# Optimization experiments

Measured on AMD Instinct MI355X. Metric: run time of the kernel, lower is better.

Reference implementation:

```python
import jax, jax.numpy as jnp
import numpy as np

B, D, R, E, L = 16384, 1024, 64, 4, 3


def setup_inputs() -> dict:
    key = jax.random.key(0)
    ks = jax.random.split(key, 6)
    x0 = jax.random.normal(ks[0], (B, D), dtype=jnp.float32)
    # Expert low-rank factors: U projects D->R, V projects R->D (both bias-free)
    U = jax.random.normal(ks[1], (L, E, D, R), dtype=jnp.float32) * (1.0 / np.sqrt(D))
    V = jax.random.normal(ks[2], (L, E, R, D), dtype=jnp.float32) * (1.0 / np.sqrt(R))
    # Gate Linear(D, E) with bias
    gW = jax.random.normal(ks[3], (L, D, E), dtype=jnp.float32) * (1.0 / np.sqrt(D))
    gb = jax.random.normal(ks[4], (L, E), dtype=jnp.float32) * 0.01
    # Per-layer bias added after mixing (initialized zeros in torch; small random here)
    bias = jax.random.normal(ks[5], (L, D), dtype=jnp.float32) * 0.01
    return {"x0": x0, "U": U, "V": V, "gW": gW, "gb": gb, "bias": bias}


def reference(x0, U, V, gW, gb, bias):
    x = x0
    for l in range(L):
        # batched low-rank expert MLPs: [B,D] -> [B,E,R] -> relu -> [B,E,D]
        h = jax.nn.relu(jnp.einsum('bd,edr->ber', x, U[l]))
        expert_out = jnp.einsum('ber,erd->bed', h, V[l])
        # soft gate over experts
        gate = jax.nn.softmax(x @ gW[l] + gb[l], axis=-1)  # [B,E]
        mixed = jnp.einsum('be,bed->bd', gate, expert_out)  # [B,D]
        x = x0 * mixed + bias[l] + x
    return x
```

## Files before the change

kernel.cpp:

```cpp
#include <hip/hip_runtime.h>

#define DEVI __device__ __forceinline__

typedef __bf16 bf16x8 __attribute__((ext_vector_type(8)));
typedef float f32x4 __attribute__((ext_vector_type(4)));
typedef unsigned short u16x8 __attribute__((ext_vector_type(8)));

DEVI unsigned short f2bf(float f) {
  unsigned u = __builtin_bit_cast(unsigned, f);
  u += 0x7FFFu + ((u >> 16) & 1u);
  return (unsigned short)(u >> 16);
}
DEVI float bf2f(unsigned short h) {
  return __builtin_bit_cast(float, (unsigned)h << 16);
}


__global__ __launch_bounds__(256) void cast_x0_kernel(const float* __restrict__ x,
                                                      unsigned short* __restrict__ xb) {
  int i = blockIdx.x * 256 + threadIdx.x;
  const f32x4* p = (const f32x4*)x;
  f32x4 a = p[2 * i], b = p[2 * i + 1];
  u16x8 o;
  o[0] = f2bf(a[0]); o[1] = f2bf(a[1]); o[2] = f2bf(a[2]); o[3] = f2bf(a[3]);
  o[4] = f2bf(b[0]); o[5] = f2bf(b[1]); o[6] = f2bf(b[2]); o[7] = f2bf(b[3]);
  ((u16x8*)xb)[i] = o;
}

__global__ __launch_bounds__(256) void pack_w1_kernel(const float* __restrict__ U,
                                                      unsigned short* __restrict__ W1T) {
  int idx = blockIdx.x * 256 + threadIdx.x;
  int l = idx >> 18;
  int rem = idx & 262143;
  int n = rem >> 10, k = rem & 1023;
  int e = n >> 6, r = n & 63;
  W1T[idx] = f2bf(U[(size_t)(((l * 4 + e) << 10) + k) * 64 + r]);
}

__global__ __launch_bounds__(256) void pack_v2_kernel(const float* __restrict__ V,
                                                      unsigned short* __restrict__ V2T) {
  int idx = blockIdx.x * 256 + threadIdx.x;
  int l = idx >> 18;
  int rem = idx & 262143;
  int d = rem >> 8, c = rem & 255;
  int e = c >> 6, r = c & 63;
  V2T[idx] = f2bf(V[(size_t)(((l * 4 + e) * 64 + r) << 10) + d]);
}

__global__ __launch_bounds__(256) void pack_gw_kernel(const float* __restrict__ gW,
                                                      unsigned short* __restrict__ gWT) {
  int idx = blockIdx.x * 256 + threadIdx.x;
  int l = idx >> 14;
  int n = (idx >> 10) & 15;
  int k = idx & 1023;
  float v = (n < 4) ? gW[l * 4096 + k * 4 + n] : 0.0f;
  gWT[idx] = f2bf(v);
}

__global__ __launch_bounds__(256) void k1_kernel(const unsigned short* __restrict__ A,
                                                 const unsigned short* __restrict__ Bw,
                                                 const unsigned short* __restrict__ gWT,
                                                 const float* __restrict__ gb,
                                                 unsigned short* __restrict__ Hg) {
  constexpr int K = 1024;
  __shared__ char lds[20480];
  __shared__ float gls[128];
  int t = threadIdx.x;
  int wid = t >> 6, lane = t & 63;
  int g4 = lane >> 4, l15 = lane & 15;
  int wm = wid >> 1, wn = wid & 1;
  int m0 = blockIdx.x * 32, n0 = blockIdx.y * 128;

  int srow = t >> 3;
  int scolb = ((t & 7) * 16) ^ ((srow & 7) << 4);
  const unsigned short* Asrc = A + (size_t)(m0 + srow) * K + (scolb >> 1);
  const unsigned short* Bsrc = Bw + (size_t)(n0 + srow) * K + (scolb >> 1);

  f32x4 acc[4], accg;
  {
    f32x4 z = {0.f, 0.f, 0.f, 0.f};
    accg = z;
#pragma unroll
    for (int n = 0; n < 4; ++n) acc[n] = z;
  }

  for (int ks = 0; ks < K; ks += 64) {
    __syncthreads();
    __builtin_amdgcn_global_load_lds(
        (const __attribute__((address_space(1))) void*)(Asrc + ks),
        (__attribute__((address_space(3))) void*)(lds + wid * 1024), 16, 0, 0);
#pragma unroll
    for (int i = 0; i < 4; ++i)
      __builtin_amdgcn_global_load_lds(
          (const __attribute__((address_space(1))) void*)(Bsrc + (size_t)i * 32 * K + ks),
          (__attribute__((address_space(3))) void*)(lds + 4096 + i * 4096 + wid * 1024), 16, 0, 0);
    __syncthreads();
#pragma unroll
    for (int kk = 0; kk < 2; ++kk) {
      bf16x8 af;
      {
        int row = wm * 16 + l15;
        af = *(const bf16x8*)(lds + row * 128 + ((kk * 64 + g4 * 16) ^ ((row & 7) << 4)));
      }
      bf16x8 gf;
      if (wn == 0) gf = *(const bf16x8*)(gWT + (size_t)l15 * 1024 + ks + kk * 32 + g4 * 8);
#pragma unroll
      for (int n = 0; n < 4; ++n) {
        int row = wn * 64 + n * 16 + l15;
        bf16x8 bfr = *(const bf16x8*)(lds + 4096 + row * 128 +
                                      ((kk * 64 + g4 * 16) ^ ((row & 7) << 4)));
        acc[n] = __builtin_amdgcn_mfma_f32_16x16x32_bf16(af, bfr, acc[n], 0, 0, 0);
      }
      if (wn == 0)
        accg = __builtin_amdgcn_mfma_f32_16x16x32_bf16(af, gf, accg, 0, 0, 0);
    }
  }

  if (wn == 0) {
    float gbv = gb[l15 & 3];
#pragma unroll
    for (int j = 0; j < 4; ++j) {
      float v = accg[j] + gbv;
      float mx = fmaxf(v, __shfl_xor(v, 1));
      mx = fmaxf(mx, __shfl_xor(mx, 2));
      float ev = __expf(v - mx);
      float s = ev + __shfl_xor(ev, 1);
      s += __shfl_xor(s, 2);
      if (l15 < 4) gls[(wm * 16 + g4 * 4 + j) * 4 + l15] = ev / s;
    }
  }
  __syncthreads();

  int e = blockIdx.y * 2 + wn;
#pragma unroll
  for (int n = 0; n < 4; ++n) {
#pragma unroll
    for (int j = 0; j < 4; ++j) {
      int row = wm * 16 + g4 * 4 + j;
      int col = wn * 64 + n * 16 + l15;
      float v = fmaxf(acc[n][j], 0.f) * gls[row * 4 + e];
      *(unsigned short*)(lds + 4096 + row * 256 + ((col * 2) ^ ((row & 7) << 4))) = f2bf(v);
    }
  }
  __syncthreads();

#pragma unroll
  for (int i = 0; i < 2; ++i) {
    int row = i * 16 + (t >> 4);
    int seg = (t & 15) * 16;
    u16x8 v = *(const u16x8*)(lds + 4096 + row * 256 + (seg ^ ((row & 7) << 4)));
    *(u16x8*)(Hg + (size_t)(m0 + row) * 256 + n0 + (seg >> 1)) = v;
  }
}

__global__ __launch_bounds__(256) void k2_kernel(const unsigned short* __restrict__ A,
                                                 const unsigned short* __restrict__ Bw,
                                                 const unsigned short* __restrict__ x0b,
                                                 const float* __restrict__ x0f,
                                                 const unsigned short* __restrict__ xcur,
                                                 const float* __restrict__ biasl,
                                                 unsigned short* __restrict__ xnext,
                                                 float* __restrict__ out,
                                                 int last, int use_x0b) {
  constexpr int K = 256;
  __shared__ char lds[24576];
  int t = threadIdx.x;
  int wid = t >> 6, lane = t & 63;
  int g4 = lane >> 4, l15 = lane & 15;
  int wm = wid >> 1, wn = wid & 1;
  int m0 = blockIdx.x * 64, n0 = blockIdx.y * 128;

  int srow = t >> 3;
  int scolb = ((t & 7) * 16) ^ ((srow & 7) << 4);
  const unsigned short* Asrc = A + (size_t)(m0 + srow) * K + (scolb >> 1);
  const unsigned short* Bsrc = Bw + (size_t)(n0 + srow) * K + (scolb >> 1);

  f32x4 acc[2][4];
#pragma unroll
  for (int m = 0; m < 2; ++m)
#pragma unroll
    for (int n = 0; n < 4; ++n) { f32x4 z = {0.f, 0.f, 0.f, 0.f}; acc[m][n] = z; }

  for (int ks = 0; ks < K; ks += 64) {
    __syncthreads();
#pragma unroll
    for (int i = 0; i < 2; ++i)
      __builtin_amdgcn_global_load_lds(
          (const __attribute__((address_space(1))) void*)(Asrc + (size_t)i * 32 * K + ks),
          (__attribute__((address_space(3))) void*)(lds + i * 4096 + wid * 1024), 16, 0, 0);
#pragma unroll
    for (int i = 0; i < 4; ++i)
      __builtin_amdgcn_global_load_lds(
          (const __attribute__((address_space(1))) void*)(Bsrc + (size_t)i * 32 * K + ks),
          (__attribute__((address_space(3))) void*)(lds + 8192 + i * 4096 + wid * 1024), 16, 0, 0);
    __syncthreads();
#pragma unroll
    for (int kk = 0; kk < 2; ++kk) {
      bf16x8 af[2];
#pragma unroll
      for (int m = 0; m < 2; ++m) {
        int row = wm * 32 + m * 16 + l15;
        af[m] = *(const bf16x8*)(lds + row * 128 + ((kk * 64 + g4 * 16) ^ ((row & 7) << 4)));
      }
#pragma unroll
      for (int n = 0; n < 4; ++n) {
        int row = wn * 64 + n * 16 + l15;
        bf16x8 bfr = *(const bf16x8*)(lds + 8192 + row * 128 +
                                      ((kk * 64 + g4 * 16) ^ ((row & 7) << 4)));
#pragma unroll
        for (int m = 0; m < 2; ++m)
          acc[m][n] = __builtin_amdgcn_mfma_f32_16x16x32_bf16(af[m], bfr, acc[m][n], 0, 0, 0);
      }
    }
  }
  __syncthreads();

#pragma unroll
  for (int m = 0; m < 2; ++m) {
#pragma unroll
    for (int n = 0; n < 4; ++n) {
#pragma unroll
      for (int j = 0; j < 4; ++j) {
        int row = wm * 32 + m * 16 + g4 * 4 + j;
        int col = wn * 64 + n * 16 + l15;
        *(unsigned short*)(lds + 8192 + row * 256 + ((col * 2) ^ ((row & 7) << 4))) =
            f2bf(acc[m][n][j]);
      }
    }
  }
  __syncthreads();

#pragma unroll
  for (int i = 0; i < 4; ++i) {
    int row = i * 16 + (t >> 4);
    int seg = (t & 15) * 16;
    u16x8 a8 = *(const u16x8*)(lds + 8192 + row * 256 + (seg ^ ((row & 7) << 4)));
    size_t goff = (size_t)(m0 + row) * 1024 + n0 + (seg >> 1);
    u16x8 cv = *(const u16x8*)(xcur + goff);
    float x0v[8];
    if (use_x0b) {
      u16x8 xv = *(const u16x8*)(x0b + goff);
#pragma unroll
      for (int k = 0; k < 8; ++k) x0v[k] = bf2f(xv[k]);
    } else {
      f32x4 xa = *(const f32x4*)(x0f + goff);
      f32x4 xb2 = *(const f32x4*)(x0f + goff + 4);
#pragma unroll
      for (int k = 0; k < 4; ++k) { x0v[k] = xa[k]; x0v[k + 4] = xb2[k]; }
    }
    const float* bp = biasl + n0 + (seg >> 1);
    f32x4 b0 = *(const f32x4*)bp;
    f32x4 b1 = *(const f32x4*)(bp + 4);
    float r[8];
#pragma unroll
    for (int k = 0; k < 8; ++k) {
      float bv = (k < 4) ? b0[k & 3] : b1[k & 3];
      r[k] = x0v[k] * bf2f(a8[k]) + bv + bf2f(cv[k]);
    }
    if (last) {
      f32x4 r0, r1;
#pragma unroll
      for (int k = 0; k < 4; ++k) { r0[k] = r[k]; r1[k] = r[k + 4]; }
      *(f32x4*)(out + goff) = r0;
      *(f32x4*)(out + goff + 4) = r1;
    } else {
      u16x8 o;
#pragma unroll
      for (int k = 0; k < 8; ++k) o[k] = f2bf(r[k]);
      *(u16x8*)(xnext + goff) = o;
    }
  }
}

extern "C" void kernel_launch(void* const* d_in, const int* in_sizes, int n_in,
                              void* d_out, int out_size, void* d_ws, size_t ws_size,
                              hipStream_t stream) {
  const float* x0 = (const float*)d_in[0];
  const float* U = (const float*)d_in[1];
  const float* V = (const float*)d_in[2];
  const float* gW = (const float*)d_in[3];
  const float* gb = (const float*)d_in[4];
  const float* bias = (const float*)d_in[5];
  float* out = (float*)d_out;
  char* ws = (char*)d_ws;

  const size_t SZ_X = 33554432;
  const size_t SZ_HG = 8388608;
  const size_t SZ_W = 1572864;
  const size_t SZ_GW = 98304;
  bool use_x0b = ws_size >= (2 * SZ_X + SZ_HG + 2 * SZ_W + SZ_GW);

  size_t off = 0;
  unsigned short* x0b = nullptr;
  if (use_x0b) { x0b = (unsigned short*)(ws + off); off += SZ_X; }
  unsigned short* xbf = (unsigned short*)(ws + off); off += SZ_X;
  unsigned short* hg = (unsigned short*)(ws + off); off += SZ_HG;
  unsigned short* W1T = (unsigned short*)(ws + off); off += SZ_W;
  unsigned short* V2T = (unsigned short*)(ws + off); off += SZ_W;
  unsigned short* gWT = (unsigned short*)(ws + off); off += SZ_GW;

  unsigned short* xinit = use_x0b ? x0b : xbf;

  cast_x0_kernel<<<8192, 256, 0, stream>>>(x0, xinit);
  pack_w1_kernel<<<3072, 256, 0, stream>>>(U, W1T);
  pack_v2_kernel<<<3072, 256, 0, stream>>>(V, V2T);
  pack_gw_kernel<<<192, 256, 0, stream>>>(gW, gWT);

  for (int l = 0; l < 3; ++l) {
    const unsigned short* xs = (l == 0) ? xinit : xbf;
    k1_kernel<<<dim3(512, 2), 256, 0, stream>>>(xs, W1T + l * 262144, gWT + l * 16384,
                                                gb + l * 4, hg);
    k2_kernel<<<dim3(256, 8), 256, 0, stream>>>(hg, V2T + l * 262144,
                                                use_x0b ? x0b : nullptr, x0, xs,
                                                bias + l * 1024, xbf, out,
                                                (l == 2) ? 1 : 0, use_x0b ? 1 : 0);
  }
}
```

Before: 180.8 us.

## Retile k1 to cover all 256 columns per block and shrink k2 M tile

k1 now gives each block all 256 output columns (4 experts × 64 rank), one expert per wave. The A tile of x is then loaded once per 32-row tile instead of twice, and the gate GEMM and softmax run once per row tile instead of per column half. k2 is cut from 64-row to 32-row tiles, which doubles its grid to spread the small-K GEMM and epilogue across more blocks. The trade-off is that k1 needs more LDS and has half as many blocks, while k2 reloads the V weights more often.

```diff
diff --git a/kernel.cpp b/kernel.cpp
--- a/kernel.cpp
+++ b/kernel.cpp
@@ -63,25 +63,25 @@
                                                  const float* __restrict__ gb,
                                                  unsigned short* __restrict__ Hg) {
   constexpr int K = 1024;
-  __shared__ char lds[20480];
+  __shared__ char lds[36864];
   __shared__ float gls[128];
   int t = threadIdx.x;
   int wid = t >> 6, lane = t & 63;
   int g4 = lane >> 4, l15 = lane & 15;
-  int wm = wid >> 1, wn = wid & 1;
-  int m0 = blockIdx.x * 32, n0 = blockIdx.y * 128;
+  int m0 = blockIdx.x * 32;
 
   int srow = t >> 3;
   int scolb = ((t & 7) * 16) ^ ((srow & 7) << 4);
   const unsigned short* Asrc = A + (size_t)(m0 + srow) * K + (scolb >> 1);
-  const unsigned short* Bsrc = Bw + (size_t)(n0 + srow) * K + (scolb >> 1);
-
-  f32x4 acc[4], accg;
-  {
+  const unsigned short* Bsrc = Bw + (size_t)srow * K + (scolb >> 1);
+
+  f32x4 acc[2][4], accg[2];
+#pragma unroll
+  for (int m = 0; m < 2; ++m) {
     f32x4 z = {0.f, 0.f, 0.f, 0.f};
-    accg = z;
-#pragma unroll
-    for (int n = 0; n < 4; ++n) acc[n] = z;
+    accg[m] = z;
+#pragma unroll
+    for (int n = 0; n < 4; ++n) acc[m][n] = z;
   }
 
   for (int ks = 0; ks < K; ks += 64) {
@@ -90,66 +90,77 @@
         (const __attribute__((address_space(1))) void*)(Asrc + ks),
         (__attribute__((address_space(3))) void*)(lds + wid * 1024), 16, 0, 0);
 #pragma unroll
-    for (int i = 0; i < 4; ++i)
+    for (int i = 0; i < 8; ++i)
       __builtin_amdgcn_global_load_lds(
           (const __attribute__((address_space(1))) void*)(Bsrc + (size_t)i * 32 * K + ks),
           (__attribute__((address_space(3))) void*)(lds + 4096 + i * 4096 + wid * 1024), 16, 0, 0);
     __syncthreads();
 #pragma unroll
     for (int kk = 0; kk < 2; ++kk) {
-      bf16x8 af;
-      {
-        int row = wm * 16 + l15;
-        af = *(const bf16x8*)(lds + row * 128 + ((kk * 64 + g4 * 16) ^ ((row & 7) << 4)));
+      bf16x8 af[2];
+#pragma unroll
+      for (int m = 0; m < 2; ++m) {
+        int row = m * 16 + l15;
+        af[m] = *(const bf16x8*)(lds + row * 128 + ((kk * 64 + g4 * 16) ^ ((row & 7) << 4)));
       }
       bf16x8 gf;
-      if (wn == 0) gf = *(const bf16x8*)(gWT + (size_t)l15 * 1024 + ks + kk * 32 + g4 * 8);
+      if (wid == 0) gf = *(const bf16x8*)(gWT + (size_t)l15 * 1024 + ks + kk * 32 + g4 * 8);
 #pragma unroll
       for (int n = 0; n < 4; ++n) {
-        int row = wn * 64 + n * 16 + l15;
+        int row = wid * 64 + n * 16 + l15;
         bf16x8 bfr = *(const bf16x8*)(lds + 4096 + row * 128 +
                                       ((kk * 64 + g4 * 16) ^ ((row & 7) << 4)));
-        acc[n] = __builtin_amdgcn_mfma_f32_16x16x32_bf16(af, bfr, acc[n], 0, 0, 0);
-      }
-      if (wn == 0)
-        accg = __builtin_amdgcn_mfma_f32_16x16x32_bf16(af, gf, accg, 0, 0, 0);
-    }
-  }
-
-  if (wn == 0) {
+#pragma unroll
+        for (int m = 0; m < 2; ++m)
+          acc[m][n] = __builtin_amdgcn_mfma_f32_16x16x32_bf16(af[m], bfr, acc[m][n], 0, 0, 0);
+      }
+      if (wid == 0) {
+#pragma unroll
+        for (int m = 0; m < 2; ++m)
+          accg[m] = __builtin_amdgcn_mfma_f32_16x16x32_bf16(af[m], gf, accg[m], 0, 0, 0);
+      }
+    }
+  }
+
+  if (wid == 0) {
     float gbv = gb[l15 & 3];
 #pragma unroll
-    for (int j = 0; j < 4; ++j) {
-      float v = accg[j] + gbv;
-      float mx = fmaxf(v, __shfl_xor(v, 1));
-      mx = fmaxf(mx, __shfl_xor(mx, 2));
-      float ev = __expf(v - mx);
-      float s = ev + __shfl_xor(ev, 1);
-      s += __shfl_xor(s, 2);
-      if (l15 < 4) gls[(wm * 16 + g4 * 4 + j) * 4 + l15] = ev / s;
+    for (int m = 0; m < 2; ++m) {
+#pragma unroll
+      for (int j = 0; j < 4; ++j) {
+        float v = accg[m][j] + gbv;
+        float mx = fmaxf(v, __shfl_xor(v, 1));
+        mx = fmaxf(mx, __shfl_xor(mx, 2));
+        float ev = __expf(v - mx);
+        float s = ev + __shfl_xor(ev, 1);
+        s += __shfl_xor(s, 2);
+        if (l15 < 4) gls[(m * 16 + g4 * 4 + j) * 4 + l15] = ev / s;
+      }
     }
   }
   __syncthreads();
 
-  int e = blockIdx.y * 2 + wn;
-#pragma unroll
-  for (int n = 0; n < 4; ++n) {
-#pragma unroll
-    for (int j = 0; j < 4; ++j) {
-      int row = wm * 16 + g4 * 4 + j;
-      int col = wn * 64 + n * 16 + l15;
-      float v = fmaxf(acc[n][j], 0.f) * gls[row * 4 + e];
-      *(unsigned short*)(lds + 4096 + row * 256 + ((col * 2) ^ ((row & 7) << 4))) = f2bf(v);
+#pragma unroll
+  for (int m = 0; m < 2; ++m) {
+#pragma unroll
+    for (int n = 0; n < 4; ++n) {
+#pragma unroll
+      for (int j = 0; j < 4; ++j) {
+        int row = m * 16 + g4 * 4 + j;
+        int col = wid * 64 + n * 16 + l15;
+        float v = fmaxf(acc[m][n][j], 0.f) * gls[row * 4 + wid];
+        *(unsigned short*)(lds + 4096 + row * 512 + ((col * 2) ^ ((row & 7) << 4))) = f2bf(v);
+      }
     }
   }
   __syncthreads();
 
 #pragma unroll
-  for (int i = 0; i < 2; ++i) {
-    int row = i * 16 + (t >> 4);
-    int seg = (t & 15) * 16;
-    u16x8 v = *(const u16x8*)(lds + 4096 + row * 256 + (seg ^ ((row & 7) << 4)));
-    *(u16x8*)(Hg + (size_t)(m0 + row) * 256 + n0 + (seg >> 1)) = v;
+  for (int i = 0; i < 4; ++i) {
+    int row = i * 8 + (t >> 5);
+    int seg = (t & 31) * 16;
+    u16x8 v = *(const u16x8*)(lds + 4096 + row * 512 + (seg ^ ((row & 7) << 4)));
+    *(u16x8*)(Hg + (size_t)(m0 + row) * 256 + (seg >> 1)) = v;
   }
 }
 
@@ -163,78 +174,68 @@
                                                  float* __restrict__ out,
                                                  int last, int use_x0b) {
   constexpr int K = 256;
-  __shared__ char lds[24576];
+  __shared__ char lds[20480];
   int t = threadIdx.x;
   int wid = t >> 6, lane = t & 63;
   int g4 = lane >> 4, l15 = lane & 15;
   int wm = wid >> 1, wn = wid & 1;
-  int m0 = blockIdx.x * 64, n0 = blockIdx.y * 128;
+  int m0 = blockIdx.x * 32, n0 = blockIdx.y * 128;
 
   int srow = t >> 3;
   int scolb = ((t & 7) * 16) ^ ((srow & 7) << 4);
   const unsigned short* Asrc = A + (size_t)(m0 + srow) * K + (scolb >> 1);
   const unsigned short* Bsrc = Bw + (size_t)(n0 + srow) * K + (scolb >> 1);
 
-  f32x4 acc[2][4];
-#pragma unroll
-  for (int m = 0; m < 2; ++m)
-#pragma unroll
-    for (int n = 0; n < 4; ++n) { f32x4 z = {0.f, 0.f, 0.f, 0.f}; acc[m][n] = z; }
+  f32x4 acc[4];
+#pragma unroll
+  for (int n = 0; n < 4; ++n) { f32x4 z = {0.f, 0.f, 0.f, 0.f}; acc[n] = z; }
 
   for (int ks = 0; ks < K; ks += 64) {
     __syncthreads();
-#pragma unroll
-    for (int i = 0; i < 2; ++i)
-      __builtin_amdgcn_global_load_lds(
-          (const __attribute__((address_space(1))) void*)(Asrc + (size_t)i * 32 * K + ks),
-          (__attribute__((address_space(3))) void*)(lds + i * 4096 + wid * 1024), 16, 0, 0);
+    __builtin_amdgcn_global_load_lds(
+        (const __attribute__((address_space(1))) void*)(Asrc + ks),
+        (__attribute__((address_space(3))) void*)(lds + wid * 1024), 16, 0, 0);
 #pragma unroll
     for (int i = 0; i < 4; ++i)
       __builtin_amdgcn_global_load_lds(
           (const __attribute__((address_space(1))) void*)(Bsrc + (size_t)i * 32 * K + ks),
-          (__attribute__((address_space(3))) void*)(lds + 8192 + i * 4096 + wid * 1024), 16, 0, 0);
+          (__attribute__((address_space(3))) void*)(lds + 4096 + i * 4096 + wid * 1024), 16, 0, 0);
     __syncthreads();
 #pragma unroll
     for (int kk = 0; kk < 2; ++kk) {
-      bf16x8 af[2];
-#pragma unroll
-      for (int m = 0; m < 2; ++m) {
-        int row = wm * 32 + m * 16 + l15;
-        af[m] = *(const bf16x8*)(lds + row * 128 + ((kk * 64 + g4 * 16) ^ ((row & 7) << 4)));
+      bf16x8 af;
+      {
+        int row = wm * 16 + l15;
+        af = *(const bf16x8*)(lds + row * 128 + ((kk * 64 + g4 * 16) ^ ((row & 7) << 4)));
       }
 #pragma unroll
       for (int n = 0; n < 4; ++n) {
         int row = wn * 64 + n * 16 + l15;
-        bf16x8 bfr = *(const bf16x8*)(lds + 8192 + row * 128 +
+        bf16x8 bfr = *(const bf16x8*)(lds + 4096 + row * 128 +
                                       ((kk * 64 + g4 * 16) ^ ((row & 7) << 4)));
-#pragma unroll
-        for (int m = 0; m < 2; ++m)
-          acc[m][n] = __builtin_amdgcn_mfma_f32_16x16x32_bf16(af[m], bfr, acc[m][n], 0, 0, 0);
+        acc[n] = __builtin_amdgcn_mfma_f32_16x16x32_bf16(af, bfr, acc[n], 0, 0, 0);
       }
     }
   }
   __syncthreads();
 
 #pragma unroll
-  for (int m = 0; m < 2; ++m) {
-#pragma unroll
-    for (int n = 0; n < 4; ++n) {
-#pragma unroll
-      for (int j = 0; j < 4; ++j) {
-        int row = wm * 32 + m * 16 + g4 * 4 + j;
-        int col = wn * 64 + n * 16 + l15;
-        *(unsigned short*)(lds + 8192 + row * 256 + ((col * 2) ^ ((row & 7) << 4))) =
-            f2bf(acc[m][n][j]);
-      }
+  for (int n = 0; n < 4; ++n) {
+#pragma unroll
+    for (int j = 0; j < 4; ++j) {
+      int row = wm * 16 + g4 * 4 + j;
+      int col = wn * 64 + n * 16 + l15;
+      *(unsigned short*)(lds + 4096 + row * 256 + ((col * 2) ^ ((row & 7) << 4))) =
+          f2bf(acc[n][j]);
     }
   }
   __syncthreads();
 
 #pragma unroll
-  for (int i = 0; i < 4; ++i) {
+  for (int i = 0; i < 2; ++i) {
     int row = i * 16 + (t >> 4);
     int seg = (t & 15) * 16;
-    u16x8 a8 = *(const u16x8*)(lds + 8192 + row * 256 + (seg ^ ((row & 7) << 4)));
+    u16x8 a8 = *(const u16x8*)(lds + 4096 + row * 256 + (seg ^ ((row & 7) << 4)));
     size_t goff = (size_t)(m0 + row) * 1024 + n0 + (seg >> 1);
     u16x8 cv = *(const u16x8*)(xcur + goff);
     float x0v[8];
@@ -248,7 +249,7 @@
 #pragma unroll
       for (int k = 0; k < 4; ++k) { x0v[k] = xa[k]; x0v[k + 4] = xb2[k]; }
     }
-    const float* bp = biasl + n0 + (seg >> 1);
+    const float* bp = biasl + n0 + ((seg >> 1));
     f32x4 b0 = *(const f32x4*)bp;
     f32x4 b1 = *(const f32x4*)(bp + 4);
     float r[8];
@@ -308,9 +309,9 @@
 
   for (int l = 0; l < 3; ++l) {
     const unsigned short* xs = (l == 0) ? xinit : xbf;
-    k1_kernel<<<dim3(512, 2), 256, 0, stream>>>(xs, W1T + l * 262144, gWT + l * 16384,
-                                                gb + l * 4, hg);
-    k2_kernel<<<dim3(256, 8), 256, 0, stream>>>(hg, V2T + l * 262144,
+    k1_kernel<<<512, 256, 0, stream>>>(xs, W1T + l * 262144, gWT + l * 16384,
+                                       gb + l * 4, hg);
+    k2_kernel<<<dim3(512, 8), 256, 0, stream>>>(hg, V2T + l * 262144,
                                                 use_x0b ? x0b : nullptr, x0, xs,
                                                 bias + l * 1024, xbf, out,
                                                 (l == 2) ? 1 : 0, use_x0b ? 1 : 0);
```

Result: slower. 185.3 us (+2.5%).

## Load k2 operands straight to registers and retile to 32x256 blocks

Applied to the files above, without the earlier changes.

The second GEMM kernel no longer stages A and B tiles through LDS with global_load_lds and block-wide barriers. Each wave keeps its full 32-row K=256 slice of the gated hidden activations in registers and streams V2T fragments directly from global memory into MFMAs. The block tile changes from 64x128 to 32x256 with per-wave 64-column strips, which removes the main-loop synchronisation and shrinks LDS use. In exchange it raises register pressure and relies on L2 and L1 for reuse of V2T across blocks, with no LDS-level sharing of operands between waves.

```diff
diff --git a/kernel.cpp b/kernel.cpp
--- a/kernel.cpp
+++ b/kernel.cpp
@@ -153,8 +153,8 @@
   }
 }
 
-__global__ __launch_bounds__(256) void k2_kernel(const unsigned short* __restrict__ A,
-                                                 const unsigned short* __restrict__ Bw,
+__global__ __launch_bounds__(256) void k2_kernel(const unsigned short* __restrict__ hg,
+                                                 const unsigned short* __restrict__ V2T,
                                                  const unsigned short* __restrict__ x0b,
                                                  const float* __restrict__ x0f,
                                                  const unsigned short* __restrict__ xcur,
@@ -162,79 +162,58 @@
                                                  unsigned short* __restrict__ xnext,
                                                  float* __restrict__ out,
                                                  int last, int use_x0b) {
-  constexpr int K = 256;
-  __shared__ char lds[24576];
+  __shared__ char lds[16384];
   int t = threadIdx.x;
   int wid = t >> 6, lane = t & 63;
   int g4 = lane >> 4, l15 = lane & 15;
-  int wm = wid >> 1, wn = wid & 1;
-  int m0 = blockIdx.x * 64, n0 = blockIdx.y * 128;
-
-  int srow = t >> 3;
-  int scolb = ((t & 7) * 16) ^ ((srow & 7) << 4);
-  const unsigned short* Asrc = A + (size_t)(m0 + srow) * K + (scolb >> 1);
-  const unsigned short* Bsrc = Bw + (size_t)(n0 + srow) * K + (scolb >> 1);
+  int m0 = blockIdx.y * 32;
+  int n0 = blockIdx.x * 256 + wid * 64;
+
+  bf16x8 a[2][8];
+#pragma unroll
+  for (int mm = 0; mm < 2; ++mm) {
+    const unsigned short* ar = hg + (size_t)(m0 + mm * 16 + l15) * 256 + g4 * 8;
+#pragma unroll
+    for (int kc = 0; kc < 8; ++kc) a[mm][kc] = *(const bf16x8*)(ar + kc * 32);
+  }
 
   f32x4 acc[2][4];
 #pragma unroll
-  for (int m = 0; m < 2; ++m)
-#pragma unroll
-    for (int n = 0; n < 4; ++n) { f32x4 z = {0.f, 0.f, 0.f, 0.f}; acc[m][n] = z; }
-
-  for (int ks = 0; ks < K; ks += 64) {
-    __syncthreads();
-#pragma unroll
-    for (int i = 0; i < 2; ++i)
-      __builtin_amdgcn_global_load_lds(
-          (const __attribute__((address_space(1))) void*)(Asrc + (size_t)i * 32 * K + ks),
-          (__attribute__((address_space(3))) void*)(lds + i * 4096 + wid * 1024), 16, 0, 0);
-#pragma unroll
-    for (int i = 0; i < 4; ++i)
-      __builtin_amdgcn_global_load_lds(
-          (const __attribute__((address_space(1))) void*)(Bsrc + (size_t)i * 32 * K + ks),
-          (__attribute__((address_space(3))) void*)(lds + 8192 + i * 4096 + wid * 1024), 16, 0, 0);
-    __syncthreads();
-#pragma unroll
-    for (int kk = 0; kk < 2; ++kk) {
-      bf16x8 af[2];
-#pragma unroll
-      for (int m = 0; m < 2; ++m) {
-        int row = wm * 32 + m * 16 + l15;
-        af[m] = *(const bf16x8*)(lds + row * 128 + ((kk * 64 + g4 * 16) ^ ((row & 7) << 4)));
+  for (int mm = 0; mm < 2; ++mm)
+#pragma unroll
+    for (int n = 0; n < 4; ++n) { f32x4 z = {0.f, 0.f, 0.f, 0.f}; acc[mm][n] = z; }
+
+#pragma unroll
+  for (int kc = 0; kc < 8; ++kc) {
+#pragma unroll
+    for (int n = 0; n < 4; ++n) {
+      bf16x8 b = *(const bf16x8*)(V2T + (size_t)(n0 + n * 16 + l15) * 256 + kc * 32 + g4 * 8);
+#pragma unroll
+      for (int mm = 0; mm < 2; ++mm)
+        acc[mm][n] = __builtin_amdgcn_mfma_f32_16x16x32_bf16(a[mm][kc], b, acc[mm][n], 0, 0, 0);
+    }
+  }
+
+  char* wlds = lds + wid * 4096;
+#pragma unroll
+  for (int mm = 0; mm < 2; ++mm) {
+#pragma unroll
+    for (int n = 0; n < 4; ++n) {
+#pragma unroll
+      for (int j = 0; j < 4; ++j) {
+        int row = mm * 16 + g4 * 4 + j;
+        int colb = (n * 16 + l15) * 2;
+        *(unsigned short*)(wlds + row * 128 + (colb ^ ((row & 3) << 5))) = f2bf(acc[mm][n][j]);
       }
-#pragma unroll
-      for (int n = 0; n < 4; ++n) {
-        int row = wn * 64 + n * 16 + l15;
-        bf16x8 bfr = *(const bf16x8*)(lds + 8192 + row * 128 +
-                                      ((kk * 64 + g4 * 16) ^ ((row & 7) << 4)));
-#pragma unroll
-        for (int m = 0; m < 2; ++m)
-          acc[m][n] = __builtin_amdgcn_mfma_f32_16x16x32_bf16(af[m], bfr, acc[m][n], 0, 0, 0);
-      }
     }
   }
   __syncthreads();
 
 #pragma unroll
-  for (int m = 0; m < 2; ++m) {
-#pragma unroll
-    for (int n = 0; n < 4; ++n) {
-#pragma unroll
-      for (int j = 0; j < 4; ++j) {
-        int row = wm * 32 + m * 16 + g4 * 4 + j;
-        int col = wn * 64 + n * 16 + l15;
-        *(unsigned short*)(lds + 8192 + row * 256 + ((col * 2) ^ ((row & 7) << 4))) =
-            f2bf(acc[m][n][j]);
-      }
-    }
-  }
-  __syncthreads();
-
-#pragma unroll
-  for (int i = 0; i < 4; ++i) {
-    int row = i * 16 + (t >> 4);
-    int seg = (t & 15) * 16;
-    u16x8 a8 = *(const u16x8*)(lds + 8192 + row * 256 + (seg ^ ((row & 7) << 4)));
+  for (int p = 0; p < 4; ++p) {
+    int row = p * 8 + (lane >> 3);
+    int seg = (lane & 7) * 16;
+    u16x8 a8 = *(const u16x8*)(wlds + row * 128 + (seg ^ ((row & 3) << 5)));
     size_t goff = (size_t)(m0 + row) * 1024 + n0 + (seg >> 1);
     u16x8 cv = *(const u16x8*)(xcur + goff);
     float x0v[8];
@@ -310,7 +289,7 @@
     const unsigned short* xs = (l == 0) ? xinit : xbf;
     k1_kernel<<<dim3(512, 2), 256, 0, stream>>>(xs, W1T + l * 262144, gWT + l * 16384,
                                                 gb + l * 4, hg);
-    k2_kernel<<<dim3(256, 8), 256, 0, stream>>>(hg, V2T + l * 262144,
+    k2_kernel<<<dim3(4, 512), 256, 0, stream>>>(hg, V2T + l * 262144,
                                                 use_x0b ? x0b : nullptr, x0, xs,
                                                 bias + l * 1024, xbf, out,
                                                 (l == 2) ? 1 : 0, use_x0b ? 1 : 0);
```

After: 284.0 us. 57.1% more time.

## Double-buffer LDS tiles in both GEMM kernels to overlap loads with MFMA

Applied to the files above, without the earlier changes.

Both GEMM main loops now use two LDS buffers. The next K-slice is issued via global_load_lds before the MFMAs on the current slice run, and there is one barrier per iteration instead of two. The aim is to hide global-to-LDS latency behind compute. In exchange, LDS per block doubles (about 40 KB and 48 KB), which can cut the number of resident blocks per CU.

```diff
diff --git a/kernel.cpp b/kernel.cpp
--- a/kernel.cpp
+++ b/kernel.cpp
@@ -63,7 +63,7 @@
                                                  const float* __restrict__ gb,
                                                  unsigned short* __restrict__ Hg) {
   constexpr int K = 1024;
-  __shared__ char lds[20480];
+  __shared__ char lds[40960];
   __shared__ float gls[128];
   int t = threadIdx.x;
   int wid = t >> 6, lane = t & 63;
@@ -84,37 +84,48 @@
     for (int n = 0; n < 4; ++n) acc[n] = z;
   }
 
-  for (int ks = 0; ks < K; ks += 64) {
-    __syncthreads();
-    __builtin_amdgcn_global_load_lds(
-        (const __attribute__((address_space(1))) void*)(Asrc + ks),
-        (__attribute__((address_space(3))) void*)(lds + wid * 1024), 16, 0, 0);
-#pragma unroll
-    for (int i = 0; i < 4; ++i)
-      __builtin_amdgcn_global_load_lds(
-          (const __attribute__((address_space(1))) void*)(Bsrc + (size_t)i * 32 * K + ks),
-          (__attribute__((address_space(3))) void*)(lds + 4096 + i * 4096 + wid * 1024), 16, 0, 0);
-    __syncthreads();
+#define K1_STAGE(b, ks)                                                                       \
+  {                                                                                           \
+    __builtin_amdgcn_global_load_lds(                                                         \
+        (const __attribute__((address_space(1))) void*)(Asrc + (ks)),                         \
+        (__attribute__((address_space(3))) void*)(lds + (b)*20480 + wid * 1024), 16, 0, 0);   \
+    _Pragma("unroll") for (int i = 0; i < 4; ++i) __builtin_amdgcn_global_load_lds(           \
+        (const __attribute__((address_space(1))) void*)(Bsrc + (size_t)i * 32 * K + (ks)),    \
+        (__attribute__((address_space(3))) void*)(lds + (b)*20480 + 4096 + i * 4096 +         \
+                                                  wid * 1024),                                \
+        16, 0, 0);                                                                            \
+  }
+
+  int cur = 0;
+  K1_STAGE(0, 0);
+  __syncthreads();
+
+  for (int s = 0; s < 16; ++s) {
+    if (s < 15) K1_STAGE(cur ^ 1, (s + 1) * 64);
+    const char* base = lds + cur * 20480;
 #pragma unroll
     for (int kk = 0; kk < 2; ++kk) {
       bf16x8 af;
       {
         int row = wm * 16 + l15;
-        af = *(const bf16x8*)(lds + row * 128 + ((kk * 64 + g4 * 16) ^ ((row & 7) << 4)));
+        af = *(const bf16x8*)(base + row * 128 + ((kk * 64 + g4 * 16) ^ ((row & 7) << 4)));
       }
       bf16x8 gf;
-      if (wn == 0) gf = *(const bf16x8*)(gWT + (size_t)l15 * 1024 + ks + kk * 32 + g4 * 8);
+      if (wn == 0) gf = *(const bf16x8*)(gWT + (size_t)l15 * 1024 + s * 64 + kk * 32 + g4 * 8);
 #pragma unroll
       for (int n = 0; n < 4; ++n) {
         int row = wn * 64 + n * 16 + l15;
-        bf16x8 bfr = *(const bf16x8*)(lds + 4096 + row * 128 +
+        bf16x8 bfr = *(const bf16x8*)(base + 4096 + row * 128 +
                                       ((kk * 64 + g4 * 16) ^ ((row & 7) << 4)));
         acc[n] = __builtin_amdgcn_mfma_f32_16x16x32_bf16(af, bfr, acc[n], 0, 0, 0);
       }
       if (wn == 0)
         accg = __builtin_amdgcn_mfma_f32_16x16x32_bf16(af, gf, accg, 0, 0, 0);
     }
-  }
+    __syncthreads();
+    cur ^= 1;
+  }
+#undef K1_STAGE
 
   if (wn == 0) {
     float gbv = gb[l15 & 3];
@@ -163,7 +174,7 @@
                                                  float* __restrict__ out,
                                                  int last, int use_x0b) {
   constexpr int K = 256;
-  __shared__ char lds[24576];
+  __shared__ char lds[49152];
   int t = threadIdx.x;
   int wid = t >> 6, lane = t & 63;
   int g4 = lane >> 4, l15 = lane & 15;
@@ -181,39 +192,48 @@
 #pragma unroll
     for (int n = 0; n < 4; ++n) { f32x4 z = {0.f, 0.f, 0.f, 0.f}; acc[m][n] = z; }
 
-  for (int ks = 0; ks < K; ks += 64) {
-    __syncthreads();
-#pragma unroll
-    for (int i = 0; i < 2; ++i)
-      __builtin_amdgcn_global_load_lds(
-          (const __attribute__((address_space(1))) void*)(Asrc + (size_t)i * 32 * K + ks),
-          (__attribute__((address_space(3))) void*)(lds + i * 4096 + wid * 1024), 16, 0, 0);
-#pragma unroll
-    for (int i = 0; i < 4; ++i)
-      __builtin_amdgcn_global_load_lds(
-          (const __attribute__((address_space(1))) void*)(Bsrc + (size_t)i * 32 * K + ks),
-          (__attribute__((address_space(3))) void*)(lds + 8192 + i * 4096 + wid * 1024), 16, 0, 0);
-    __syncthreads();
+#define K2_STAGE(b, ks)                                                                       \
+  {                                                                                           \
+    _Pragma("unroll") for (int i = 0; i < 2; ++i) __builtin_amdgcn_global_load_lds(           \
+        (const __attribute__((address_space(1))) void*)(Asrc + (size_t)i * 32 * K + (ks)),    \
+        (__attribute__((address_space(3))) void*)(lds + (b)*24576 + i * 4096 + wid * 1024),   \
+        16, 0, 0);                                                                            \
+    _Pragma("unroll") for (int i = 0; i < 4; ++i) __builtin_amdgcn_global_load_lds(           \
+        (const __attribute__((address_space(1))) void*)(Bsrc + (size_t)i * 32 * K + (ks)),    \
+        (__attribute__((address_space(3))) void*)(lds + (b)*24576 + 8192 + i * 4096 +         \
+                                                  wid * 1024),                                \
+        16, 0, 0);                                                                            \
+  }
+
+  int cur = 0;
+  K2_STAGE(0, 0);
+  __syncthreads();
+
+  for (int s = 0; s < 4; ++s) {
+    if (s < 3) K2_STAGE(cur ^ 1, (s + 1) * 64);
+    const char* base = lds + cur * 24576;
 #pragma unroll
     for (int kk = 0; kk < 2; ++kk) {
       bf16x8 af[2];
 #pragma unroll
       for (int m = 0; m < 2; ++m) {
         int row = wm * 32 + m * 16 + l15;
-        af[m] = *(const bf16x8*)(lds + row * 128 + ((kk * 64 + g4 * 16) ^ ((row & 7) << 4)));
+        af[m] = *(const bf16x8*)(base + row * 128 + ((kk * 64 + g4 * 16) ^ ((row & 7) << 4)));
       }
 #pragma unroll
       for (int n = 0; n < 4; ++n) {
         int row = wn * 64 + n * 16 + l15;
-        bf16x8 bfr = *(const bf16x8*)(lds + 8192 + row * 128 +
+        bf16x8 bfr = *(const bf16x8*)(base + 8192 + row * 128 +
                                       ((kk * 64 + g4 * 16) ^ ((row & 7) << 4)));
 #pragma unroll
         for (int m = 0; m < 2; ++m)
           acc[m][n] = __builtin_amdgcn_mfma_f32_16x16x32_bf16(af[m], bfr, acc[m][n], 0, 0, 0);
       }
     }
-  }
-  __syncthreads();
+    __syncthreads();
+    cur ^= 1;
+  }
+#undef K2_STAGE
 
 #pragma unroll
   for (int m = 0; m < 2; ++m) {
```

After: 219.5 us. 21.4% more time.
